# Optimization experiments

Measured on AMD Instinct MI355X. Metric: run time of the kernel, lower is better.

Reference implementation:

```python
import jax, jax.numpy as jnp
import numpy as np

B, MBS, F, CD = 512, 32768, 512, 16  # batch, mini_batch_size, filter_length, cond_dim

def setup_inputs() -> dict:
    key = jax.random.key(0)
    ks = jax.random.split(key, 8)
    return {
        "inputs": jax.random.normal(ks[0], (B, MBS, 1), jnp.float32),
        "c": jax.random.normal(ks[1], (B, 1, CD), jnp.float32),
        "W0": jax.random.normal(ks[2], (CD, F), jnp.float32) * 0.1,
        "b0": jnp.zeros((F,), jnp.float32),
        "alpha": jnp.full((F,), 0.25, jnp.float32),
        "Wg": jax.random.normal(ks[3], (CD, F), jnp.float32) * 0.1,
        "bg": jnp.zeros((F,), jnp.float32),
        "Wb": jax.random.normal(ks[4], (CD, F), jnp.float32) * 0.1,
        "bb": jnp.zeros((F,), jnp.float32),
        "Wglu": jax.random.normal(ks[5], (F, 2 * F), jnp.float32) * 0.05,
        "bglu": jnp.zeros((2 * F,), jnp.float32),
        "Wf": jax.random.normal(ks[6], (F, F), jnp.float32) * 0.05,
        "bf": jnp.zeros((F,), jnp.float32),
    }

def reference(inputs, c, W0, b0, alpha, Wg, bg, Wb, bb, Wglu, bglu, Wf, bf):
    mbs = inputs.shape[1]
    flen = Wf.shape[1]
    # conditioning stack: Dense -> PReLU -> FiLM -> GLU -> Dense(softsign)
    c_ = c @ W0 + b0                                  # [B,1,F]
    c_ = jnp.where(c_ >= 0, c_, alpha * c_)           # PReLU
    c_ = c_ * (c @ Wg + bg) + (c @ Wb + bb)           # FiLM
    g = c_ @ Wglu + bglu                              # [B,1,2F]
    a, gate = jnp.split(g, 2, axis=-1)
    c_ = a * jax.nn.sigmoid(gate)                     # GLU
    filters = jax.nn.soft_sign(c_ @ Wf + bf)          # [B,1,F]
    # FFT-based circular (linear via zero pad) convolution
    conv_len = mbs + flen - 1
    X = jnp.fft.fft(inputs[:, :, 0].astype(jnp.complex64), n=conv_len)   # [B,conv_len]
    H = jnp.fft.fft(filters[:, 0, :].astype(jnp.complex64), n=conv_len)  # [B,conv_len]
    y = jnp.fft.ifft(X * H)
    return jnp.real(y[:, :mbs])                       # [B,MBS]
```

## Files before the change

kernel.cpp:

```cpp
#include <hip/hip_runtime.h>


typedef float f32x16 __attribute__((ext_vector_type(16)));
typedef float f32x4  __attribute__((ext_vector_type(4)));
typedef __bf16 bf16x8 __attribute__((ext_vector_type(8)));

__device__ __forceinline__ unsigned short f2bf(float f) {
    unsigned int u = __float_as_uint(f);
    u += 0x7FFFu + ((u >> 16) & 1u);
    return (unsigned short)(u >> 16);
}

__device__ __forceinline__ uint4 pack8n(float4 a, float4 b) {
    bf16x8 v;
    v[0] = (__bf16)a.x; v[1] = (__bf16)a.y; v[2] = (__bf16)a.z; v[3] = (__bf16)a.w;
    v[4] = (__bf16)b.x; v[5] = (__bf16)b.y; v[6] = (__bf16)b.z; v[7] = (__bf16)b.w;
    uint4 r;
    __builtin_memcpy(&r, &v, 16);
    return r;
}

__global__ __launch_bounds__(256) void kA(
    const float* __restrict__ Wglu, const float* __restrict__ Wf,
    const float* __restrict__ c, const float* __restrict__ W0,
    const float* __restrict__ b0, const float* __restrict__ alpha,
    const float* __restrict__ Wg, const float* __restrict__ bg,
    const float* __restrict__ Wb, const float* __restrict__ bb,
    unsigned short* __restrict__ WgluT, unsigned short* __restrict__ WfT,
    unsigned short* __restrict__ cfilm) {
    const int blk = blockIdx.x, tid = threadIdx.x;
    if (blk < 192) {
        __shared__ float ldsF[64 * 65];
        const float* src; unsigned short* dst; int tj, tk, srcld;
        if (blk < 128) { tj = blk >> 3; tk = blk & 7; src = Wglu; dst = WgluT; srcld = 1024; }
        else { int b2 = blk - 128; tj = b2 >> 3; tk = b2 & 7; src = Wf; dst = WfT; srcld = 512; }
#pragma unroll
        for (int rr = 0; rr < 16; ++rr) {
            int kl = (tid >> 6) + (rr << 2), jl = tid & 63;
            ldsF[kl * 65 + jl] = src[(size_t)(tk * 64 + kl) * srcld + tj * 64 + jl];
        }
        __syncthreads();
#pragma unroll
        for (int rr = 0; rr < 16; ++rr) {
            int jl = (tid >> 6) + (rr << 2), kl = tid & 63;
            dst[(size_t)(tj * 64 + jl) * 512 + tk * 64 + kl] = f2bf(ldsF[kl * 65 + jl]);
        }
    } else {
        int id = (blk - 192) * 256 + tid;
        int b = id >> 9, f = id & 511;
        const float* cb = c + b * 16;
        float d0 = 0.f, dg = 0.f, db = 0.f;
#pragma unroll
        for (int i = 0; i < 16; ++i) {
            float cv = cb[i];
            d0 += cv * W0[i * 512 + f];
            dg += cv * Wg[i * 512 + f];
            db += cv * Wb[i * 512 + f];
        }
        float pre = d0 + b0[f];
        float pr = pre >= 0.f ? pre : alpha[f] * pre;
        float v = pr * (dg + bg[f]) + (db + bb[f]);
        cfilm[id] = f2bf(v);
    }
}

__global__ __launch_bounds__(256) void k2_glu(
    const unsigned short* __restrict__ cfilm, const unsigned short* __restrict__ WgluT,
    const float* __restrict__ bglu, unsigned short* __restrict__ cglu) {
    int wid = (blockIdx.x * 256 + threadIdx.x) >> 6;
    int l = threadIdx.x & 63;
    int tm = wid >> 5, tn = wid & 31;
    int row = tm * 16 + (l & 15);
    int col = tn * 16 + (l & 15);
    int kh = 8 * (l >> 4);
    f32x4 accA, accG;
#pragma unroll
    for (int i = 0; i < 4; ++i) { accA[i] = 0.f; accG[i] = 0.f; }
    const unsigned short* ap  = cfilm + row * 512 + kh;
    const unsigned short* bap = WgluT + col * 512 + kh;
    const unsigned short* bgp = WgluT + (512 + col) * 512 + kh;
#pragma unroll
    for (int kc = 0; kc < 16; ++kc) {
        bf16x8 a   = *(const bf16x8*)(ap  + kc * 32);
        bf16x8 ba  = *(const bf16x8*)(bap + kc * 32);
        bf16x8 bgt = *(const bf16x8*)(bgp + kc * 32);
        accA = __builtin_amdgcn_mfma_f32_16x16x32_bf16(a, ba,  accA, 0, 0, 0);
        accG = __builtin_amdgcn_mfma_f32_16x16x32_bf16(a, bgt, accG, 0, 0, 0);
    }
    float biasA = bglu[col], biasG = bglu[512 + col];
#pragma unroll
    for (int r = 0; r < 4; ++r) {
        float ga = accA[r] + biasA;
        float gg = accG[r] + biasG;
        float s = 1.f / (1.f + expf(-gg));
        int m = (l >> 4) * 4 + r;
        cglu[(tm * 16 + m) * 512 + col] = f2bf(ga * s);
    }
}

__global__ __launch_bounds__(256) void k3_filt(
    const unsigned short* __restrict__ cglu, const unsigned short* __restrict__ WfT,
    const float* __restrict__ bfv, unsigned short* __restrict__ hout) {
    int wid = (blockIdx.x * 256 + threadIdx.x) >> 6;
    int l = threadIdx.x & 63;
    int tm = wid >> 5, tn = wid & 31;
    int row = tm * 16 + (l & 15);
    int col = tn * 16 + (l & 15);
    int kh = 8 * (l >> 4);
    f32x4 acc;
#pragma unroll
    for (int i = 0; i < 4; ++i) acc[i] = 0.f;
    const unsigned short* ap = cglu + row * 512 + kh;
    const unsigned short* bp = WfT + col * 512 + kh;
#pragma unroll
    for (int kc = 0; kc < 16; ++kc) {
        bf16x8 a  = *(const bf16x8*)(ap + kc * 32);
        bf16x8 bv = *(const bf16x8*)(bp + kc * 32);
        acc = __builtin_amdgcn_mfma_f32_16x16x32_bf16(a, bv, acc, 0, 0, 0);
    }
    float bias = bfv[col];
#pragma unroll
    for (int r = 0; r < 4; ++r) {
        float z = acc[r] + bias;
        float h = z / (1.f + fabsf(z));
        int m = (l >> 4) * 4 + r;
        hout[(tm * 16 + m) * 512 + col] = f2bf(h);
    }
}

__global__ __launch_bounds__(256, 4) void k6(
    const float* __restrict__ x, const unsigned short* __restrict__ hbf,
    float* __restrict__ y) {
    __shared__ __align__(16) unsigned char smem[28800];
    const int tid = threadIdx.x;
    const int b = blockIdx.x >> 1;
    const int n0 = (blockIdx.x & 1) << 14;
    const float* xb = x + (size_t)b * 32768;
    unsigned short* hs = (unsigned short*)(smem + 27776);

    ((unsigned int*)hs)[tid] = ((const unsigned int*)(hbf + (size_t)b * 512))[tid];
    __syncthreads();

    for (int e = tid; e < 8 * 292; e += 256) {
        int s = e / 292, w = e - s * 292;
        int j0 = 2 * w + s;
        unsigned int v0 = (j0 >= 32 && j0 < 544) ? hs[543 - j0] : 0u;
        unsigned int v1 = (j0 >= 31 && j0 < 543) ? hs[542 - j0] : 0u;
        ((unsigned int*)(smem + 18432))[e] = v0 | (v1 << 16);
    }

#pragma unroll
    for (int r2 = 0; r2 < 3; ++r2) {
        int slot = tid + (r2 << 8);
        if (slot < 576) {
            int off = n0 + ((slot - 64) << 3);
            uint4 w4;
            if (off >= 0) {
                float4 a  = *(const float4*)(xb + off);
                float4 b2 = *(const float4*)(xb + off + 4);
                w4 = pack8n(a, b2);
            } else {
                w4 = make_uint4(0u, 0u, 0u, 0u);
            }
            *(uint4*)(smem + ((slot ^ ((slot >> 3) & 7)) << 4)) = w4;
        }
    }
    __syncthreads();

    const int w = tid >> 6, l = tid & 63;
    const int q = l & 31, hl = l >> 5;
    const int lq = 4 * q + hl;
    const int abase = 66 + (w << 7) + lq;
    const int o0 = 559 - q + 8 * hl;
    const int s8 = o0 & 7;
    const unsigned char* hrb = smem + 18432 + s8 * 1168 + ((o0 - s8) << 1);

    for (int c = 0; c < 4; ++c) {
        const unsigned char* wb = smem + ((c & 1) ? 9216 : 0);
        unsigned char* sb = smem + ((c & 1) ? 0 : 9216);
        float4 La0, Lb0, La1, Lb1, La2, Lb2;
        if (c < 3) {
            const float* px = xb + n0 + ((c + 1) << 12) - 512;
            La0 = *(const float4*)(px + (tid << 3));         Lb0 = *(const float4*)(px + (tid << 3) + 4);
            La1 = *(const float4*)(px + ((tid + 256) << 3)); Lb1 = *(const float4*)(px + ((tid + 256) << 3) + 4);
            if (tid < 64) {
                La2 = *(const float4*)(px + ((tid + 512) << 3));
                Lb2 = *(const float4*)(px + ((tid + 512) << 3) + 4);
            }
        }
        f32x16 acc;
#pragma unroll
        for (int i = 0; i < 16; ++i) acc[i] = 0.f;
#pragma unroll
        for (int cc = 0; cc < 17; ++cc) {
            bf16x8 bfr = *(const bf16x8*)(hrb - (cc << 5));
            int a0 = abase - 2 * cc;
            bf16x8 xa = *(const bf16x8*)(wb + ((a0 ^ ((a0 >> 3) & 7)) << 4));
            acc = __builtin_amdgcn_mfma_f32_32x32x16_bf16(xa, bfr, acc, 0, 0, 0);
        }
        if (c < 3) {
            int s0 = tid;
            *(uint4*)(sb + ((s0 ^ ((s0 >> 3) & 7)) << 4)) = pack8n(La0, Lb0);
            int s1 = tid + 256;
            *(uint4*)(sb + ((s1 ^ ((s1 >> 3) & 7)) << 4)) = pack8n(La1, Lb1);
            if (tid < 64) {
                int s2 = tid + 512;
                *(uint4*)(sb + ((s2 ^ ((s2 >> 3) & 7)) << 4)) = pack8n(La2, Lb2);
            }
        }
#pragma unroll
        for (int cc = 17; cc < 34; ++cc) {
            bf16x8 bfr = *(const bf16x8*)(hrb - (cc << 5));
            int a0 = abase - 2 * cc;
            bf16x8 xa = *(const bf16x8*)(wb + ((a0 ^ ((a0 >> 3) & 7)) << 4));
            acc = __builtin_amdgcn_mfma_f32_32x32x16_bf16(xa, bfr, acc, 0, 0, 0);
        }
        asm volatile("s_waitcnt lgkmcnt(0)" ::: "memory");
        __builtin_amdgcn_s_barrier();
        __builtin_amdgcn_sched_barrier(0);
        float* yb = y + (size_t)b * 32768 + n0 + (c << 12) + (w << 10) + q;
#pragma unroll
        for (int r = 0; r < 16; ++r) {
            int m = (r & 3) + 8 * (r >> 2) + 4 * hl;
            yb[m << 5] = acc[r];
        }
    }
}

extern "C" void kernel_launch(void* const* d_in, const int* in_sizes, int n_in,
                              void* d_out, int out_size, void* d_ws, size_t ws_size,
                              hipStream_t stream) {
    const float* x    = (const float*)d_in[0];
    const float* c    = (const float*)d_in[1];
    const float* W0   = (const float*)d_in[2];
    const float* b0   = (const float*)d_in[3];
    const float* al   = (const float*)d_in[4];
    const float* Wg   = (const float*)d_in[5];
    const float* bg   = (const float*)d_in[6];
    const float* Wb   = (const float*)d_in[7];
    const float* bb   = (const float*)d_in[8];
    const float* Wglu = (const float*)d_in[9];
    const float* bglu = (const float*)d_in[10];
    const float* Wf   = (const float*)d_in[11];
    const float* bf   = (const float*)d_in[12];
    float* y = (float*)d_out;

    char* ws = (char*)d_ws;
    unsigned short* cfilm = (unsigned short*)(ws);
    unsigned short* WgluT = (unsigned short*)(ws + 524288);
    unsigned short* WfT   = (unsigned short*)(ws + 1572864);
    unsigned short* cglu  = (unsigned short*)(ws + 2097152);
    unsigned short* hbf   = (unsigned short*)(ws + 2621440);

    kA<<<dim3(1216), dim3(256), 0, stream>>>(Wglu, Wf, c, W0, b0, al, Wg, bg, Wb, bb,
                                             WgluT, WfT, cfilm);
    k2_glu<<<dim3(256), dim3(256), 0, stream>>>(cfilm, WgluT, bglu, cglu);
    k3_filt<<<dim3(256), dim3(256), 0, stream>>>(cglu, WfT, bf, hbf);
    k6<<<dim3(1024), dim3(256), 0, stream>>>(x, hbf, y);
}
```

Baseline: 52.01 us.

## Split conv kernel into 2048 single-pass blocks with dual accumulators and remapped block order

The direct-convolution kernel now launches 2048 blocks, each covering an 8192-sample quarter of a batch row in one pass, where before 1024 blocks each looped over four double-buffered 4096-sample chunks. Each wave keeps two MFMA accumulators that share every filter fragment load. Block indices are permuted so that the four blocks of one batch row land apart, and the occupancy hint rises to 5 blocks per CU. This drops the in-loop prefetch and barrier pipeline in exchange for more parallelism and less LDS per block, at the cost of loading the input tile up front with no overlap and of duplicating the filter-table setup across twice as many blocks.

```diff
diff --git a/kernel.cpp b/kernel.cpp
--- a/kernel.cpp
+++ b/kernel.cpp
@@ -128,15 +128,17 @@
     }
 }
 
-__global__ __launch_bounds__(256, 4) void k6(
+__global__ __launch_bounds__(256, 5) void k7(
     const float* __restrict__ x, const unsigned short* __restrict__ hbf,
     float* __restrict__ y) {
-    __shared__ __align__(16) unsigned char smem[28800];
+    __shared__ __align__(16) unsigned char smem[27776];
     const int tid = threadIdx.x;
-    const int b = blockIdx.x >> 1;
-    const int n0 = (blockIdx.x & 1) << 14;
+    const int nb = blockIdx.x;
+    const int virt = ((nb >> 5) << 5) + ((nb & 7) << 2) + ((nb >> 3) & 3);
+    const int b = virt >> 2;
+    const int n0 = (virt & 3) << 13;
     const float* xb = x + (size_t)b * 32768;
-    unsigned short* hs = (unsigned short*)(smem + 27776);
+    unsigned short* hs = (unsigned short*)(smem + 26752);
 
     ((unsigned int*)hs)[tid] = ((const unsigned int*)(hbf + (size_t)b * 512))[tid];
     __syncthreads();
@@ -146,13 +148,13 @@
         int j0 = 2 * w + s;
         unsigned int v0 = (j0 >= 32 && j0 < 544) ? hs[543 - j0] : 0u;
         unsigned int v1 = (j0 >= 31 && j0 < 543) ? hs[542 - j0] : 0u;
-        ((unsigned int*)(smem + 18432))[e] = v0 | (v1 << 16);
-    }
-
-#pragma unroll
-    for (int r2 = 0; r2 < 3; ++r2) {
+        ((unsigned int*)(smem + 17408))[e] = v0 | (v1 << 16);
+    }
+
+#pragma unroll
+    for (int r2 = 0; r2 < 5; ++r2) {
         int slot = tid + (r2 << 8);
-        if (slot < 576) {
+        if (slot < 1088) {
             int off = n0 + ((slot - 64) << 3);
             uint4 w4;
             if (off >= 0) {
@@ -170,60 +172,29 @@
     const int w = tid >> 6, l = tid & 63;
     const int q = l & 31, hl = l >> 5;
     const int lq = 4 * q + hl;
-    const int abase = 66 + (w << 7) + lq;
+    const int abase = 66 + (w << 8) + lq;
     const int o0 = 559 - q + 8 * hl;
     const int s8 = o0 & 7;
-    const unsigned char* hrb = smem + 18432 + s8 * 1168 + ((o0 - s8) << 1);
-
-    for (int c = 0; c < 4; ++c) {
-        const unsigned char* wb = smem + ((c & 1) ? 9216 : 0);
-        unsigned char* sb = smem + ((c & 1) ? 0 : 9216);
-        float4 La0, Lb0, La1, Lb1, La2, Lb2;
-        if (c < 3) {
-            const float* px = xb + n0 + ((c + 1) << 12) - 512;
-            La0 = *(const float4*)(px + (tid << 3));         Lb0 = *(const float4*)(px + (tid << 3) + 4);
-            La1 = *(const float4*)(px + ((tid + 256) << 3)); Lb1 = *(const float4*)(px + ((tid + 256) << 3) + 4);
-            if (tid < 64) {
-                La2 = *(const float4*)(px + ((tid + 512) << 3));
-                Lb2 = *(const float4*)(px + ((tid + 512) << 3) + 4);
-            }
-        }
-        f32x16 acc;
-#pragma unroll
-        for (int i = 0; i < 16; ++i) acc[i] = 0.f;
-#pragma unroll
-        for (int cc = 0; cc < 17; ++cc) {
-            bf16x8 bfr = *(const bf16x8*)(hrb - (cc << 5));
-            int a0 = abase - 2 * cc;
-            bf16x8 xa = *(const bf16x8*)(wb + ((a0 ^ ((a0 >> 3) & 7)) << 4));
-            acc = __builtin_amdgcn_mfma_f32_32x32x16_bf16(xa, bfr, acc, 0, 0, 0);
-        }
-        if (c < 3) {
-            int s0 = tid;
-            *(uint4*)(sb + ((s0 ^ ((s0 >> 3) & 7)) << 4)) = pack8n(La0, Lb0);
-            int s1 = tid + 256;
-            *(uint4*)(sb + ((s1 ^ ((s1 >> 3) & 7)) << 4)) = pack8n(La1, Lb1);
-            if (tid < 64) {
-                int s2 = tid + 512;
-                *(uint4*)(sb + ((s2 ^ ((s2 >> 3) & 7)) << 4)) = pack8n(La2, Lb2);
-            }
-        }
-#pragma unroll
-        for (int cc = 17; cc < 34; ++cc) {
-            bf16x8 bfr = *(const bf16x8*)(hrb - (cc << 5));
-            int a0 = abase - 2 * cc;
-            bf16x8 xa = *(const bf16x8*)(wb + ((a0 ^ ((a0 >> 3) & 7)) << 4));
-            acc = __builtin_amdgcn_mfma_f32_32x32x16_bf16(xa, bfr, acc, 0, 0, 0);
-        }
-        asm volatile("s_waitcnt lgkmcnt(0)" ::: "memory");
-        __builtin_amdgcn_s_barrier();
-        __builtin_amdgcn_sched_barrier(0);
-        float* yb = y + (size_t)b * 32768 + n0 + (c << 12) + (w << 10) + q;
-#pragma unroll
-        for (int r = 0; r < 16; ++r) {
-            int m = (r & 3) + 8 * (r >> 2) + 4 * hl;
-            yb[m << 5] = acc[r];
-        }
+    const unsigned char* hrb = smem + 17408 + s8 * 1168 + ((o0 - s8) << 1);
+
+    f32x16 acc0, acc1;
+#pragma unroll
+    for (int i = 0; i < 16; ++i) { acc0[i] = 0.f; acc1[i] = 0.f; }
+#pragma unroll
+    for (int cc = 0; cc < 34; ++cc) {
+        bf16x8 bfr = *(const bf16x8*)(hrb - (cc << 5));
+        int a0 = abase - 2 * cc, a1 = a0 + 128;
+        bf16x8 xa0 = *(const bf16x8*)(smem + ((a0 ^ ((a0 >> 3) & 7)) << 4));
+        bf16x8 xa1 = *(const bf16x8*)(smem + ((a1 ^ ((a1 >> 3) & 7)) << 4));
+        acc0 = __builtin_amdgcn_mfma_f32_32x32x16_bf16(xa0, bfr, acc0, 0, 0, 0);
+        acc1 = __builtin_amdgcn_mfma_f32_32x32x16_bf16(xa1, bfr, acc1, 0, 0, 0);
+    }
+    float* yb = y + (size_t)b * 32768 + n0 + (w << 11) + q;
+#pragma unroll
+    for (int r = 0; r < 16; ++r) {
+        int m = (r & 3) + 8 * (r >> 2) + 4 * hl;
+        yb[m << 5] = acc0[r];
+        yb[1024 + (m << 5)] = acc1[r];
     }
 }
 
@@ -256,5 +227,5 @@
                                              WgluT, WfT, cfilm);
     k2_glu<<<dim3(256), dim3(256), 0, stream>>>(cfilm, WgluT, bglu, cglu);
     k3_filt<<<dim3(256), dim3(256), 0, stream>>>(cglu, WfT, bf, hbf);
-    k6<<<dim3(1024), dim3(256), 0, stream>>>(x, hbf, y);
-}
+    k7<<<dim3(2048), dim3(256), 0, stream>>>(x, hbf, y);
+}
```

Measured after the change: 52.88 us. No clear change (+1.7%).
